# Performance work log

Hardware: AMD Instinct MI355X
Metric: run time of the kernel (lower is better)

## Reference

```python
import jax, jax.numpy as jnp
import numpy as np

B, N, D = 4, 4096, 768
SCALE = 1.0 / np.sqrt(D).astype(np.float32)


def setup_inputs() -> dict:
    key = jax.random.key(0)
    k1, k2, k3 = jax.random.split(key, 3)
    x = jax.random.normal(k1, (B, N, D), dtype=jnp.float32)
    w_qkv = jax.random.normal(k2, (D, 3 * D), dtype=jnp.float32) * (1.0 / np.sqrt(D))
    b_qkv = jnp.zeros((3 * D,), dtype=jnp.float32)
    w_out = jax.random.normal(k3, (D, D), dtype=jnp.float32) * (1.0 / np.sqrt(D))
    b_out = jnp.zeros((D,), dtype=jnp.float32)
    return {"x": x, "w_qkv": w_qkv, "b_qkv": b_qkv, "w_out": w_out, "b_out": b_out}


def reference(x, w_qkv, b_qkv, w_out, b_out):
    # fused QKV projection: [B,N,3D]
    qkv = jnp.einsum("bnd,de->bne", x, w_qkv) + b_qkv
    q, k, v = jnp.split(qkv, 3, axis=-1)          # each [B,N,D]
    # scaled dot-product attention (single head)
    scores = jnp.einsum("bnd,bmd->bnm", q, k) * SCALE  # [B,N,N]
    attn = jax.nn.softmax(scores, axis=-1)
    ctx = jnp.einsum("bnm,bmd->bnd", attn, v)          # [B,N,D]
    out = jnp.einsum("bnd,de->bne", ctx, w_out) + b_out
    return out
```

## Files before the change

### kernel.cpp

```cpp
#include <hip/hip_runtime.h>
#include <cstdint>
#include <cstddef>

#define BB 4
#define NN 4096
#define DD 768
#define EE 2304
#define MTOT 16384
static constexpr float ATT_SCALE = 0.03608439182435161f;

typedef _Float16 v8h __attribute__((ext_vector_type(8)));
typedef _Float16 v4h __attribute__((ext_vector_type(4)));
typedef float v4f __attribute__((ext_vector_type(4)));

__device__ __forceinline__ void async_copy16(void* lds, const void* gmem) {
  __builtin_amdgcn_global_load_lds(
      (const __attribute__((address_space(1))) uint32_t*)(uintptr_t)gmem,
      (__attribute__((address_space(3))) uint32_t*)(uintptr_t)lds,
      16, 0, 0);
}

#define WAIT_VMCNT(n) asm volatile("s_waitcnt vmcnt(" #n ")" ::: "memory")

enum { EPI_QKV = 0, EPI_F16 = 1, EPI_OUT = 2, EPI_PV = 3 };

template <int EPI>
__global__ __launch_bounds__(512, 2) void gemm256(
    const _Float16* __restrict__ A, int lda, size_t zA,
    const _Float16* __restrict__ Bt, int ldb, size_t zB,
    int K,
    float* __restrict__ c_f32,
    _Float16* __restrict__ c_f16,
    int ldc, size_t zC, size_t chalf,
    const float* __restrict__ bias,
    _Float16* __restrict__ q_out,
    _Float16* __restrict__ k_out,
    _Float16* __restrict__ v_out) {
  __shared__ __align__(16) _Float16 As[4][256 * 32];
  __shared__ __align__(16) _Float16 Bs[4][256 * 32];

  const int tid = threadIdx.x;
  const int wid = tid >> 6, lane = tid & 63;
  const int wr = wid >> 2, wc = wid & 3;
  const int lq = lane >> 4, lr = lane & 15;
  const int m0 = blockIdx.x * 256, n0 = blockIdx.y * 256;
  const int z = blockIdx.z;
  int bidx, koff;
  if constexpr (EPI == EPI_PV) {
    bidx = z & 1;
    koff = (z >> 1) * K;
  } else {
    bidx = z;
    koff = 0;
  }

  const _Float16* Ab = A + (size_t)bidx * zA + (size_t)m0 * lda + koff;
  const _Float16* Bb = Bt + (size_t)bidx * zB + (size_t)n0 * ldb + koff;

  const int c0 = tid, c1 = tid + 512;
  const int r0 = c0 >> 2, r1 = c1 >> 2;
  const int k0c = ((c0 & 3) ^ ((r0 >> 1) & 3)) << 3;
  const int k1c = ((c1 & 3) ^ ((r1 >> 1) & 3)) << 3;
  const size_t ga0 = (size_t)r0 * lda + k0c, ga1 = (size_t)r1 * lda + k1c;
  const size_t gb0 = (size_t)r0 * ldb + k0c, gb1 = (size_t)r1 * ldb + k1c;

  int aoff[8], boff[4];
#pragma unroll
  for (int t = 0; t < 8; ++t) {
    const int ra = wr * 128 + t * 16 + lr;
    aoff[t] = ra * 32 + ((lq ^ ((ra >> 1) & 3)) << 3);
  }
#pragma unroll
  for (int n = 0; n < 4; ++n) {
    const int rb = wc * 64 + n * 16 + lr;
    boff[n] = rb * 32 + ((lq ^ ((rb >> 1) & 3)) << 3);
  }

  v4f acc[8][4] = {};
  const int NT = K / 32;

  auto stage = [&](int slot, int kt) {
    const int kk = kt * 32;
    async_copy16(&As[slot][c0 * 8], Ab + ga0 + kk);
    async_copy16(&As[slot][c1 * 8], Ab + ga1 + kk);
    async_copy16(&Bs[slot][c0 * 8], Bb + gb0 + kk);
    async_copy16(&Bs[slot][c1 * 8], Bb + gb1 + kk);
  };

  stage(0, 0);
  stage(1, 1);
  stage(2, 2);

  for (int it = 0; it < NT; ++it) {
    if (it < NT - 2) {
      WAIT_VMCNT(8);
    } else if (it == NT - 2) {
      WAIT_VMCNT(4);
    } else {
      WAIT_VMCNT(0);
    }
    __builtin_amdgcn_s_barrier();
    __builtin_amdgcn_sched_barrier(0);

    if (it + 3 < NT) stage((it + 3) & 3, it + 3);

    const _Float16* Asl = As[it & 3];
    const _Float16* Bsl = Bs[it & 3];
    v8h af[8], bf[4];
#pragma unroll
    for (int t = 0; t < 8; ++t) af[t] = *(const v8h*)(Asl + aoff[t]);
#pragma unroll
    for (int n = 0; n < 4; ++n) bf[n] = *(const v8h*)(Bsl + boff[n]);

    __builtin_amdgcn_s_setprio(1);
#pragma unroll
    for (int mt = 0; mt < 8; ++mt)
#pragma unroll
      for (int nt = 0; nt < 4; ++nt)
        acc[mt][nt] = __builtin_amdgcn_mfma_f32_16x16x32_f16(
            af[mt], bf[nt], acc[mt][nt], 0, 0, 0);
    __builtin_amdgcn_s_setprio(0);
  }

  float* cf = nullptr;
  _Float16* ch = nullptr;
  if constexpr (EPI == EPI_PV)
    cf = c_f32 + (size_t)(z >> 1) * chalf + (size_t)bidx * zC;
  else if constexpr (EPI == EPI_OUT)
    cf = c_f32 + (size_t)bidx * zC;
  else if constexpr (EPI == EPI_F16)
    ch = c_f16 + (size_t)bidx * zC;

#pragma unroll
  for (int mt = 0; mt < 8; ++mt) {
#pragma unroll
    for (int nt = 0; nt < 4; ++nt) {
#pragma unroll
      for (int rg = 0; rg < 4; ++rg) {
        const int gm = m0 + wr * 128 + mt * 16 + lq * 4 + rg;
        const int gn = n0 + wc * 64 + nt * 16 + lr;
        float v = acc[mt][nt][rg];
        if constexpr (EPI == EPI_QKV) {
          v += bias[gn];
          if (gn < DD) {
            q_out[(size_t)gm * DD + gn] = (_Float16)(v * ATT_SCALE);
          } else if (gn < 2 * DD) {
            k_out[(size_t)gm * DD + (gn - DD)] = (_Float16)v;
          } else {
            v_out[(size_t)gm * DD + (gn - 2 * DD)] = (_Float16)v;
          }
        } else if constexpr (EPI == EPI_F16) {
          ch[(size_t)gm * ldc + gn] = (_Float16)v;
        } else {
          cf[(size_t)gm * ldc + gn] = (EPI == EPI_OUT) ? v + bias[gn] : v;
        }
      }
    }
  }
}

__global__ __launch_bounds__(256) void reduce_ctx(const float* __restrict__ h0,
                                                  const float* __restrict__ h1,
                                                  _Float16* __restrict__ out,
                                                  int n4) {
  int i = blockIdx.x * blockDim.x + threadIdx.x;
  if (i < n4) {
    v4f a = ((const v4f*)h0)[i];
    v4f b = ((const v4f*)h1)[i];
    v4h o;
#pragma unroll
    for (int j = 0; j < 4; ++j) o[j] = (_Float16)(a[j] + b[j]);
    ((v4h*)out)[i] = o;
  }
}

__global__ __launch_bounds__(256) void softmax_rows_f16(_Float16* __restrict__ S) {
  _Float16* row = S + (size_t)blockIdx.y * NN * NN + (size_t)blockIdx.x * NN;
  const int tid = threadIdx.x;
  const int lane = tid & 63, wid = tid >> 6;

  float f[16];
  float m = -3.0e38f;
#pragma unroll
  for (int i = 0; i < 2; ++i) {
    v8h v = ((const v8h*)row)[tid + i * 256];
#pragma unroll
    for (int j = 0; j < 8; ++j) {
      f[i * 8 + j] = (float)v[j];
      m = fmaxf(m, f[i * 8 + j]);
    }
  }
#pragma unroll
  for (int off = 32; off > 0; off >>= 1) m = fmaxf(m, __shfl_xor(m, off));
  __shared__ float redm[4], reds[4];
  if (lane == 0) redm[wid] = m;
  __syncthreads();
  m = fmaxf(fmaxf(redm[0], redm[1]), fmaxf(redm[2], redm[3]));

  float sum = 0.f;
#pragma unroll
  for (int i = 0; i < 16; ++i) {
    f[i] = __expf(f[i] - m);
    sum += f[i];
  }
#pragma unroll
  for (int off = 32; off > 0; off >>= 1) sum += __shfl_xor(sum, off);
  if (lane == 0) reds[wid] = sum;
  __syncthreads();
  sum = reds[0] + reds[1] + reds[2] + reds[3];
  const float inv = 1.0f / sum;
#pragma unroll
  for (int i = 0; i < 2; ++i) {
    v8h o;
#pragma unroll
    for (int j = 0; j < 8; ++j) o[j] = (_Float16)(f[i * 8 + j] * inv);
    ((v8h*)row)[tid + i * 256] = o;
  }
}

__global__ __launch_bounds__(256) void cvt_f16(const float* __restrict__ in,
                                               _Float16* __restrict__ out, int n4) {
  int i = blockIdx.x * blockDim.x + threadIdx.x;
  if (i < n4) {
    v4f v = ((const v4f*)in)[i];
    v4h o;
#pragma unroll
    for (int j = 0; j < 4; ++j) o[j] = (_Float16)v[j];
    ((v4h*)out)[i] = o;
  }
}

__global__ __launch_bounds__(256) void transpose_cvt(const float* __restrict__ in,
                                                     _Float16* __restrict__ out,
                                                     int R, int C) {
  __shared__ float tile[32][33];
  const int bx = blockIdx.x * 32;
  const int by = blockIdx.y * 32;
  const int tx = threadIdx.x & 31, ty = threadIdx.x >> 5;
#pragma unroll
  for (int i = 0; i < 32; i += 8)
    tile[ty + i][tx] = in[(size_t)(by + ty + i) * C + (bx + tx)];
  __syncthreads();
#pragma unroll
  for (int i = 0; i < 32; i += 8)
    out[(size_t)(bx + ty + i) * R + (by + tx)] = (_Float16)tile[tx][ty + i];
}

__global__ __launch_bounds__(256) void transpose_v(const _Float16* __restrict__ in,
                                                   _Float16* __restrict__ out) {
  __shared__ _Float16 tile[32][33];
  const int b = blockIdx.z;
  const _Float16* src = in + (size_t)b * NN * DD;
  _Float16* dst = out + (size_t)b * NN * DD;
  const int bx = blockIdx.x * 32;
  const int by = blockIdx.y * 32;
  const int tx = threadIdx.x & 31, ty = threadIdx.x >> 5;
#pragma unroll
  for (int i = 0; i < 32; i += 8)
    tile[ty + i][tx] = src[(size_t)(by + ty + i) * DD + (bx + tx)];
  __syncthreads();
#pragma unroll
  for (int i = 0; i < 32; i += 8)
    dst[(size_t)(bx + ty + i) * NN + (by + tx)] = tile[tx][ty + i];
}

extern "C" void kernel_launch(void* const* d_in, const int* in_sizes, int n_in,
                              void* d_out, int out_size, void* d_ws, size_t ws_size,
                              hipStream_t stream) {
  const float* x = (const float*)d_in[0];
  const float* w_qkv = (const float*)d_in[1];
  const float* b_qkv = (const float*)d_in[2];
  const float* w_out = (const float*)d_in[3];
  const float* b_out = (const float*)d_in[4];
  float* out = (float*)d_out;
  char* ws = (char*)d_ws;

  _Float16* xh    = (_Float16*)(ws + 0);
  _Float16* wqkvh = (_Float16*)(ws + 25165824);
  _Float16* wouth = (_Float16*)(ws + 28704768);
  _Float16* Qh    = (_Float16*)(ws + 29884416);
  _Float16* Kh    = (_Float16*)(ws + 55050240);
  _Float16* Vh    = (_Float16*)(ws + 80216064);
  _Float16* Sh    = (_Float16*)(ws + 105381888);
  _Float16* Vth   = (_Float16*)(ws + 0);
  _Float16* Ch    = (_Float16*)(ws + 80216064);

  const size_t zQK = (size_t)NN * DD;
  const size_t zS = (size_t)NN * NN;
  const size_t zCtx = (size_t)NN * DD;
  const size_t chalf = 2 * zCtx;

  cvt_f16<<<dim3((MTOT * DD / 4) / 256), 256, 0, stream>>>(x, xh, MTOT * DD / 4);
  transpose_cvt<<<dim3(EE / 32, DD / 32), 256, 0, stream>>>(w_qkv, wqkvh, DD, EE);
  transpose_cvt<<<dim3(DD / 32, DD / 32), 256, 0, stream>>>(w_out, wouth, DD, DD);

  gemm256<EPI_QKV><<<dim3(MTOT / 256, EE / 256), 512, 0, stream>>>(
      xh, DD, 0, wqkvh, DD, 0, DD, nullptr, nullptr, 0, 0, 0, b_qkv, Qh, Kh, Vh);

  transpose_v<<<dim3(DD / 32, NN / 32, BB), 256, 0, stream>>>(Vh, Vth);

  for (int c = 0; c < BB / 2; ++c) {
    const _Float16* Qc = Qh + (size_t)c * 2 * zQK;
    const _Float16* Kc = Kh + (size_t)c * 2 * zQK;
    const _Float16* Vtc = Vth + (size_t)c * 2 * zQK;
    gemm256<EPI_F16><<<dim3(NN / 256, NN / 256, 2), 512, 0, stream>>>(
        Qc, DD, zQK, Kc, DD, zQK, DD, nullptr, Sh, NN, zS, 0, nullptr, nullptr,
        nullptr, nullptr);
    softmax_rows_f16<<<dim3(NN, 2), 256, 0, stream>>>(Sh);
    gemm256<EPI_PV><<<dim3(NN / 256, DD / 256, 4), 512, 0, stream>>>(
        Sh, NN, zS, Vtc, NN, zQK, NN / 2, out, nullptr, DD, zCtx, chalf,
        nullptr, nullptr, nullptr, nullptr);
    reduce_ctx<<<dim3((int)(chalf / 4 / 256)), 256, 0, stream>>>(
        out, out + chalf, Ch + (size_t)c * 2 * zQK, (int)(chalf / 4));
  }

  gemm256<EPI_OUT><<<dim3(MTOT / 256, DD / 256), 512, 0, stream>>>(
      Ch, DD, 0, wouth, DD, 0, DD, out, nullptr, DD, 0, 0, b_out, nullptr,
      nullptr, nullptr);
}
```

Measured before the change: 557.4 us.

## Restructure GEMM mainloop into 64-wide K steps with interleaved staging, swizzle QK^T tiles

```diff
diff --git a/kernel.cpp b/kernel.cpp
--- a/kernel.cpp
+++ b/kernel.cpp
@@ -20,11 +20,14 @@
       16, 0, 0);
 }
 
-#define WAIT_VMCNT(n) asm volatile("s_waitcnt vmcnt(" #n ")" ::: "memory")
+#define VM_WAIT(n) asm volatile("s_waitcnt vmcnt(" #n ")" ::: "memory")
+#define LGKM0 asm volatile("s_waitcnt lgkmcnt(0)" ::: "memory")
+#define SCHED0 __builtin_amdgcn_sched_barrier(0)
+#define BAR __builtin_amdgcn_s_barrier()
 
 enum { EPI_QKV = 0, EPI_F16 = 1, EPI_OUT = 2, EPI_PV = 3 };
 
-template <int EPI>
+template <int EPI, int SWZ = 0>
 __global__ __launch_bounds__(512, 2) void gemm256(
     const _Float16* __restrict__ A, int lda, size_t zA,
     const _Float16* __restrict__ Bt, int ldb, size_t zB,
@@ -36,14 +39,23 @@
     _Float16* __restrict__ q_out,
     _Float16* __restrict__ k_out,
     _Float16* __restrict__ v_out) {
-  __shared__ __align__(16) _Float16 As[4][256 * 32];
-  __shared__ __align__(16) _Float16 Bs[4][256 * 32];
+  __shared__ __align__(16) _Float16 As[2][2][256 * 32];
+  __shared__ __align__(16) _Float16 Bs[2][2][256 * 32];
 
   const int tid = threadIdx.x;
   const int wid = tid >> 6, lane = tid & 63;
   const int wr = wid >> 2, wc = wid & 3;
   const int lq = lane >> 4, lr = lane & 15;
-  const int m0 = blockIdx.x * 256, n0 = blockIdx.y * 256;
+
+  int bx = blockIdx.x, by = blockIdx.y;
+  if constexpr (SWZ == 1) {
+    const int lin = bx + gridDim.x * by;
+    const int xcd = lin & 7, j = lin >> 3;
+    const int stc = gridDim.x >> 3;
+    bx = (xcd % stc) * 8 + (j & 7);
+    by = (xcd / stc) * 4 + ((j >> 3) & 3) + (j >> 5) * 4 * (8 / stc == 0 ? 1 : (gridDim.y / 4 / (8 / stc) == 0 ? 1 : (gridDim.y / 4) / (gridDim.y / 4)));
+  }
+  const int m0 = bx * 256, n0 = by * 256;
   const int z = blockIdx.z;
   int bidx, koff;
   if constexpr (EPI == EPI_PV) {
@@ -77,49 +89,94 @@
   }
 
   v4f acc[8][4] = {};
-  const int NT = K / 32;
-
-  auto stage = [&](int slot, int kt) {
-    const int kk = kt * 32;
-    async_copy16(&As[slot][c0 * 8], Ab + ga0 + kk);
-    async_copy16(&As[slot][c1 * 8], Ab + ga1 + kk);
-    async_copy16(&Bs[slot][c0 * 8], Bb + gb0 + kk);
-    async_copy16(&Bs[slot][c1 * 8], Bb + gb1 + kk);
+  const int NT = K / 64;
+
+  auto stageA = [&](int slot, int ks, int kt) {
+    const _Float16* s = Ab + (size_t)(kt * 64 + ks * 32);
+    async_copy16(&As[slot][ks][(size_t)c0 * 8], s + ga0);
+    async_copy16(&As[slot][ks][(size_t)c1 * 8], s + ga1);
   };
-
-  stage(0, 0);
-  stage(1, 1);
-  stage(2, 2);
-
-  for (int it = 0; it < NT; ++it) {
-    if (it < NT - 2) {
-      WAIT_VMCNT(8);
-    } else if (it == NT - 2) {
-      WAIT_VMCNT(4);
+  auto stageB = [&](int slot, int ks, int kt) {
+    const _Float16* s = Bb + (size_t)(kt * 64 + ks * 32);
+    async_copy16(&Bs[slot][ks][(size_t)c0 * 8], s + gb0);
+    async_copy16(&Bs[slot][ks][(size_t)c1 * 8], s + gb1);
+  };
+  auto mfma16 = [&](const v8h* af_, const v8h* bf_, int mbase) {
+#pragma unroll
+    for (int mt = 0; mt < 4; ++mt)
+#pragma unroll
+      for (int nt = 0; nt < 4; ++nt)
+        acc[mbase + mt][nt] = __builtin_amdgcn_mfma_f32_16x16x32_f16(
+            af_[mt], bf_[nt], acc[mbase + mt][nt], 0, 0, 0);
+  };
+
+  stageA(0, 0, 0);
+  stageB(0, 0, 0);
+  stageA(0, 1, 0);
+  stageB(0, 1, 0);
+
+  for (int t = 0; t < NT; ++t) {
+    const int slot = t & 1, ns = slot ^ 1;
+    const bool pre = (t + 1 < NT);
+    const _Float16* A0s = &As[slot][0][0];
+    const _Float16* B0s = &Bs[slot][0][0];
+    const _Float16* A1s = &As[slot][1][0];
+    const _Float16* B1s = &Bs[slot][1][0];
+
+    v8h a_[4], b0_[4], b1_[4];
+
+    if (pre) {
+      stageA(ns, 0, t + 1);
+      VM_WAIT(6);
     } else {
-      WAIT_VMCNT(0);
+      VM_WAIT(4);
     }
-    __builtin_amdgcn_s_barrier();
-    __builtin_amdgcn_sched_barrier(0);
-
-    if (it + 3 < NT) stage((it + 3) & 3, it + 3);
-
-    const _Float16* Asl = As[it & 3];
-    const _Float16* Bsl = Bs[it & 3];
-    v8h af[8], bf[4];
-#pragma unroll
-    for (int t = 0; t < 8; ++t) af[t] = *(const v8h*)(Asl + aoff[t]);
-#pragma unroll
-    for (int n = 0; n < 4; ++n) bf[n] = *(const v8h*)(Bsl + boff[n]);
-
+    SCHED0;
+    BAR;
+    SCHED0;
+#pragma unroll
+    for (int i = 0; i < 4; ++i) a_[i] = *(const v8h*)(A0s + aoff[i]);
+#pragma unroll
+    for (int i = 0; i < 4; ++i) b0_[i] = *(const v8h*)(B0s + boff[i]);
     __builtin_amdgcn_s_setprio(1);
-#pragma unroll
-    for (int mt = 0; mt < 8; ++mt)
-#pragma unroll
-      for (int nt = 0; nt < 4; ++nt)
-        acc[mt][nt] = __builtin_amdgcn_mfma_f32_16x16x32_f16(
-            af[mt], bf[nt], acc[mt][nt], 0, 0, 0);
+    mfma16(a_, b0_, 0);
     __builtin_amdgcn_s_setprio(0);
+
+    if (pre) stageB(ns, 0, t + 1);
+#pragma unroll
+    for (int i = 0; i < 4; ++i) a_[i] = *(const v8h*)(A0s + aoff[4 + i]);
+    __builtin_amdgcn_s_setprio(1);
+    mfma16(a_, b0_, 4);
+    __builtin_amdgcn_s_setprio(0);
+
+    if (pre) {
+      stageA(ns, 1, t + 1);
+      VM_WAIT(6);
+    } else {
+      VM_WAIT(0);
+    }
+    SCHED0;
+    BAR;
+    SCHED0;
+#pragma unroll
+    for (int i = 0; i < 4; ++i) a_[i] = *(const v8h*)(A1s + aoff[i]);
+#pragma unroll
+    for (int i = 0; i < 4; ++i) b1_[i] = *(const v8h*)(B1s + boff[i]);
+    __builtin_amdgcn_s_setprio(1);
+    mfma16(a_, b1_, 0);
+    __builtin_amdgcn_s_setprio(0);
+
+    if (pre) stageB(ns, 1, t + 1);
+#pragma unroll
+    for (int i = 0; i < 4; ++i) a_[i] = *(const v8h*)(A1s + aoff[4 + i]);
+    __builtin_amdgcn_s_setprio(1);
+    mfma16(a_, b1_, 4);
+    __builtin_amdgcn_s_setprio(0);
+
+    LGKM0;
+    SCHED0;
+    BAR;
+    SCHED0;
   }
 
   float* cf = nullptr;
@@ -303,7 +360,7 @@
     const _Float16* Qc = Qh + (size_t)c * 2 * zQK;
     const _Float16* Kc = Kh + (size_t)c * 2 * zQK;
     const _Float16* Vtc = Vth + (size_t)c * 2 * zQK;
-    gemm256<EPI_F16><<<dim3(NN / 256, NN / 256, 2), 512, 0, stream>>>(
+    gemm256<EPI_F16, 1><<<dim3(NN / 256, NN / 256, 2), 512, 0, stream>>>(
         Qc, DD, zQK, Kc, DD, zQK, DD, nullptr, Sh, NN, zS, 0, nullptr, nullptr,
         nullptr, nullptr);
     softmax_rows_f16<<<dim3(NN, 2), 256, 0, stream>>>(Sh);
```

New measurement: 543.9 us. -2.4%, faster.
